# Kernel tuning notes

Measured on AMD Instinct MI355X. Metric: run time of the kernel, lower is better.

## Reference

```python
import jax, jax.numpy as jnp
import numpy as np

B = 16384       # batch of weight blocks
IN = 64         # input_size == e_dim
DENC = 512      # dim_encoder
NRES = 2        # n_resblock (weights shared, see ResidualStack [block]*n)
NE = 2048       # n_embeddings
P = 12          # basis vectors per block
BETA = 0.25
SCALE = 1.0
SHIFT = 0.0


def setup_inputs() -> dict:
    key = jax.random.key(0)
    ks = jax.random.split(key, 6)
    s = 0.02
    return {
        "x": jax.random.normal(ks[0], (B, IN), dtype=jnp.float32),
        "enc_w1": jax.random.normal(ks[1], (IN, DENC), dtype=jnp.float32) * s,
        "enc_b1": jnp.zeros((DENC,), jnp.float32),
        "res_w": jax.random.normal(ks[2], (DENC, DENC), dtype=jnp.float32) * s,
        "res_b": jnp.zeros((DENC,), jnp.float32),
        "res_g": jnp.ones((DENC,), jnp.float32),
        "res_beta": jnp.zeros((DENC,), jnp.float32),
        "enc_w2": jax.random.normal(ks[3], (DENC, IN * P), dtype=jnp.float32) * s,
        "enc_b2": jnp.zeros((IN * P,), jnp.float32),
        "emb": jax.random.uniform(ks[4], (NE, IN), jnp.float32, -1.0 / NE, 1.0 / NE),
    }


def _layer_norm(r, g, b):
    mu = jnp.mean(r, axis=-1, keepdims=True)
    var = jnp.mean((r - mu) ** 2, axis=-1, keepdims=True)
    return (r - mu) * jax.lax.rsqrt(var + 1e-5) * g + b


def reference(x, enc_w1, enc_b1, res_w, res_b, res_g, res_beta, enc_w2, enc_b2, emb):
    sg = jax.lax.stop_gradient
    x_shift = (x - SHIFT) / SCALE

    # encoder: Linear -> (shared ResBlock) x NRES -> Linear
    h = x_shift @ enc_w1 + enc_b1                      # (B, DENC)
    for _ in range(NRES):
        h = h + jax.nn.relu(_layer_norm(h @ res_w + res_b, res_g, res_beta))
    z = h @ enc_w2 + enc_b2                            # (B, P*IN)

    z_e = z.reshape(B, P, IN)
    zf = z_e.reshape(-1, IN)                           # (B*P, IN)

    # pairwise squared distances to codebook, argmin, gather
    d = (jnp.sum(zf ** 2, axis=1, keepdims=True)
         + jnp.sum(emb ** 2, axis=1)
         - 2.0 * zf @ emb.T)                           # (B*P, NE)
    idx = jnp.argmin(d, axis=1)                        # (B*P,)
    z_q = emb[idx].reshape(B, P, IN)

    loss = (jnp.mean((sg(z_q) - z_e) ** 2)
            + BETA * jnp.mean((z_q - sg(z_e)) ** 2))

    # straight-through estimator
    z_q = z_e + sg(z_q - z_e)

    counts = jnp.zeros((NE,), jnp.float32).at[idx].add(1.0) / idx.shape[0]
    perplexity = jnp.exp(-jnp.sum(counts * jnp.log(counts + 1e-10)))

    # pinv-based reconstruction: A (B, IN, P), coeff = pinv(A) @ x_shift
    A = jnp.transpose(z_q, (0, 2, 1))                  # (B, IN, P)
    coeff = jnp.matmul(jnp.linalg.pinv(A), x_shift[..., None])  # (B, P, 1)
    x_hat = jnp.matmul(A, coeff)[..., 0]               # (B, IN)
    x_hat = SCALE * x_hat + SHIFT

    return (loss, x_hat, perplexity, idx, coeff)
```

## Files before the change

kernel.cpp:

```cpp
#include <hip/hip_runtime.h>
#include <math.h>

#define B_    16384
#define IN_   64
#define DENC_ 512
#define NE_   2048
#define P_    12
#define ROWS_ 196608
#define BETA_ 0.25

#define XHAT_OFF 1
#define PERP_OFF 1048577
#define IDXF_OFF 1048578
#define COEF_OFF 1245186

typedef __bf16 bf16x8 __attribute__((ext_vector_type(8)));
typedef float  f32x16 __attribute__((ext_vector_type(16)));

__device__ __forceinline__ void split3(float v, __bf16& h, __bf16& m, __bf16& l) {
    h = (__bf16)v;
    float r1 = v - (float)h;
    m = (__bf16)r1;
    float r2 = r1 - (float)m;
    l = (__bf16)r2;
}

__global__ void k_wsplit(const float* __restrict__ W,
                         __bf16* __restrict__ Wh, __bf16* __restrict__ Wm,
                         __bf16* __restrict__ Wl, int kshift, int N, int total) {
    int idx = blockIdx.x * 256 + threadIdx.x;
    if (idx < total) {
        int n = idx >> kshift;
        int k = idx & ((1 << kshift) - 1);
        float v = W[(size_t)k * N + n];
        __bf16 h, m, l;
        split3(v, h, m, l);
        Wh[idx] = h; Wm[idx] = m; Wl[idx] = l;
    }
}

__global__ __launch_bounds__(256) void k_gemm_mfma(const float* __restrict__ A,
                                                   const __bf16* __restrict__ Bh,
                                                   const __bf16* __restrict__ Bm,
                                                   const __bf16* __restrict__ Bl,
                                                   const float* __restrict__ bias,
                                                   float* __restrict__ C,
                                                   int N, int K) {
    __shared__ __bf16 eS[3][64 * 64];

    const int tid = threadIdx.x;
    const int w = tid >> 6, lane = tid & 63;
    const int r0 = blockIdx.y * 128 + w * 32;
    const int n0 = blockIdx.x * 64;
    const int lrow = lane & 31;
    const int half = lane >> 5;

    f32x16 acc0, acc1;
#pragma unroll
    for (int i = 0; i < 16; ++i) { acc0[i] = 0.0f; acc1[i] = 0.0f; }

    for (int k0 = 0; k0 < K; k0 += 64) {
        __syncthreads();
        {
            const int col = tid >> 3, q = tid & 7;
#pragma unroll
            for (int p = 0; p < 2; ++p) {
                int cc = col + 32 * p;
                int g = q ^ (cc & 7);
                size_t soff = (size_t)(n0 + cc) * K + k0 + q * 8;
                int doff = cc * 64 + g * 8;
                *(float4*)(&eS[0][doff]) = *(const float4*)(Bh + soff);
                *(float4*)(&eS[1][doff]) = *(const float4*)(Bm + soff);
                *(float4*)(&eS[2][doff]) = *(const float4*)(Bl + soff);
            }
        }
        __syncthreads();

        bf16x8 ah[4], am[4], al[4];
        {
            const float* ar = A + (size_t)(r0 + lrow) * K + k0 + half * 8;
#pragma unroll
            for (int kc = 0; kc < 4; ++kc) {
                float4 u0 = *(const float4*)(ar + kc * 16);
                float4 u1 = *(const float4*)(ar + kc * 16 + 4);
                float v[8] = {u0.x, u0.y, u0.z, u0.w, u1.x, u1.y, u1.z, u1.w};
#pragma unroll
                for (int j = 0; j < 8; ++j) {
                    __bf16 hh, mm, ll;
                    split3(v[j], hh, mm, ll);
                    ah[kc][j] = hh; am[kc][j] = mm; al[kc][j] = ll;
                }
            }
        }

#pragma unroll
        for (int kc = 0; kc < 4; ++kc) {
            const int q = kc * 2 + half;
            const int g = (q ^ (lrow & 7)) * 8;
            bf16x8 b0h = *(const bf16x8*)(&eS[0][lrow * 64 + g]);
            bf16x8 b0m = *(const bf16x8*)(&eS[1][lrow * 64 + g]);
            bf16x8 b0l = *(const bf16x8*)(&eS[2][lrow * 64 + g]);
            bf16x8 b1h = *(const bf16x8*)(&eS[0][(lrow + 32) * 64 + g]);
            bf16x8 b1m = *(const bf16x8*)(&eS[1][(lrow + 32) * 64 + g]);
            bf16x8 b1l = *(const bf16x8*)(&eS[2][(lrow + 32) * 64 + g]);

            acc0 = __builtin_amdgcn_mfma_f32_32x32x16_bf16(ah[kc], b0h, acc0, 0, 0, 0);
            acc1 = __builtin_amdgcn_mfma_f32_32x32x16_bf16(ah[kc], b1h, acc1, 0, 0, 0);
            acc0 = __builtin_amdgcn_mfma_f32_32x32x16_bf16(ah[kc], b0m, acc0, 0, 0, 0);
            acc1 = __builtin_amdgcn_mfma_f32_32x32x16_bf16(ah[kc], b1m, acc1, 0, 0, 0);
            acc0 = __builtin_amdgcn_mfma_f32_32x32x16_bf16(am[kc], b0h, acc0, 0, 0, 0);
            acc1 = __builtin_amdgcn_mfma_f32_32x32x16_bf16(am[kc], b1h, acc1, 0, 0, 0);
            acc0 = __builtin_amdgcn_mfma_f32_32x32x16_bf16(ah[kc], b0l, acc0, 0, 0, 0);
            acc1 = __builtin_amdgcn_mfma_f32_32x32x16_bf16(ah[kc], b1l, acc1, 0, 0, 0);
            acc0 = __builtin_amdgcn_mfma_f32_32x32x16_bf16(am[kc], b0m, acc0, 0, 0, 0);
            acc1 = __builtin_amdgcn_mfma_f32_32x32x16_bf16(am[kc], b1m, acc1, 0, 0, 0);
            acc0 = __builtin_amdgcn_mfma_f32_32x32x16_bf16(al[kc], b0h, acc0, 0, 0, 0);
            acc1 = __builtin_amdgcn_mfma_f32_32x32x16_bf16(al[kc], b1h, acc1, 0, 0, 0);
        }
    }

    const int col0 = n0 + lrow, col1 = col0 + 32;
    const float bv0 = bias[col0], bv1 = bias[col1];
#pragma unroll
    for (int r = 0; r < 16; ++r) {
        int row = r0 + (r & 3) + 8 * (r >> 2) + 4 * half;
        C[(size_t)row * N + col0] = acc0[r] + bv0;
        C[(size_t)row * N + col1] = acc1[r] + bv1;
    }
}

__global__ __launch_bounds__(256) void k_lnrelu(const float* __restrict__ t,
                                                float* __restrict__ h,
                                                const float* __restrict__ g,
                                                const float* __restrict__ beta) {
    const int tid = threadIdx.x;
    const int wv = tid >> 6, lane = tid & 63;
    const int row = blockIdx.x * 4 + wv;
    const float* tr = t + (size_t)row * DENC_;
    float* hr = h + (size_t)row * DENC_;

    float4 v0 = *(const float4*)(tr + lane * 4);
    float4 v1 = *(const float4*)(tr + 256 + lane * 4);

    float s = v0.x + v0.y + v0.z + v0.w + v1.x + v1.y + v1.z + v1.w;
#pragma unroll
    for (int m = 1; m < 64; m <<= 1) s += __shfl_xor(s, m);
    float mu = s / 512.0f;

    float d0x = v0.x - mu, d0y = v0.y - mu, d0z = v0.z - mu, d0w = v0.w - mu;
    float d1x = v1.x - mu, d1y = v1.y - mu, d1z = v1.z - mu, d1w = v1.w - mu;
    float vs = d0x * d0x + d0y * d0y + d0z * d0z + d0w * d0w +
               d1x * d1x + d1y * d1y + d1z * d1z + d1w * d1w;
#pragma unroll
    for (int m = 1; m < 64; m <<= 1) vs += __shfl_xor(vs, m);
    float var = vs / 512.0f;
    float rs = (float)(1.0 / sqrt((double)var + 1e-5));

    float4 g0 = *(const float4*)(g + lane * 4);
    float4 g1 = *(const float4*)(g + 256 + lane * 4);
    float4 b0 = *(const float4*)(beta + lane * 4);
    float4 b1 = *(const float4*)(beta + 256 + lane * 4);

    float4 h0 = *(float4*)(hr + lane * 4);
    float4 h1 = *(float4*)(hr + 256 + lane * 4);

    h0.x += fmaxf(d0x * rs * g0.x + b0.x, 0.0f);
    h0.y += fmaxf(d0y * rs * g0.y + b0.y, 0.0f);
    h0.z += fmaxf(d0z * rs * g0.z + b0.z, 0.0f);
    h0.w += fmaxf(d0w * rs * g0.w + b0.w, 0.0f);
    h1.x += fmaxf(d1x * rs * g1.x + b1.x, 0.0f);
    h1.y += fmaxf(d1y * rs * g1.y + b1.y, 0.0f);
    h1.z += fmaxf(d1z * rs * g1.z + b1.z, 0.0f);
    h1.w += fmaxf(d1w * rs * g1.w + b1.w, 0.0f);

    *(float4*)(hr + lane * 4) = h0;
    *(float4*)(hr + 256 + lane * 4) = h1;
}

__global__ void k_esplit(const float* __restrict__ emb, float* __restrict__ se,
                         __bf16* __restrict__ Ehi, __bf16* __restrict__ Emid,
                         __bf16* __restrict__ Elo) {
    int c = blockIdx.x * 256 + threadIdx.x;
    if (c < NE_) {
        float s = 0.0f;
        for (int k = 0; k < 64; ++k) {
            float v = emb[(size_t)c * 64 + k];
            s += v * v;
            __bf16 h, m, l;
            split3(v, h, m, l);
            Ehi[(size_t)c * 64 + k] = h;
            Emid[(size_t)c * 64 + k] = m;
            Elo[(size_t)c * 64 + k] = l;
        }
        se[c] = s;
    }
}

__global__ __launch_bounds__(256) void k_rowsq(const float* __restrict__ z,
                                               float* __restrict__ sz) {
    const int tid = threadIdx.x;
    const int row = blockIdx.x * 64 + (tid >> 2);
    const int part = tid & 3;
    const float4* zp = (const float4*)(z + (size_t)row * 64) + part * 4;
    float s = 0.0f;
#pragma unroll
    for (int i = 0; i < 4; ++i) {
        float4 v = zp[i];
        s += v.x * v.x + v.y * v.y + v.z * v.z + v.w * v.w;
    }
    s += __shfl_xor(s, 1);
    s += __shfl_xor(s, 2);
    if (part == 0) sz[row] = s;
}

__global__ __launch_bounds__(256) void k_distm(const float* __restrict__ z,
                                               const float* __restrict__ se,
                                               const float* __restrict__ sz,
                                               const __bf16* __restrict__ Ehi,
                                               const __bf16* __restrict__ Emid,
                                               const __bf16* __restrict__ Elo,
                                               int* __restrict__ idxw,
                                               float* __restrict__ idxf,
                                               float* __restrict__ dminw,
                                               int* __restrict__ counts) {
    __shared__ __bf16 eS[3][64 * 64];

    const int tid = threadIdx.x;
    const int w = tid >> 6, lane = tid & 63;
    const int r0 = blockIdx.x * 128 + w * 32;
    const int lrow = lane & 31;
    const int half = lane >> 5;

    bf16x8 ah[4], am[4], al[4];
    {
        const float* zr = z + (size_t)(r0 + lrow) * 64 + half * 8;
#pragma unroll
        for (int kc = 0; kc < 4; ++kc) {
            float4 u0 = *(const float4*)(zr + kc * 16);
            float4 u1 = *(const float4*)(zr + kc * 16 + 4);
            float v[8] = {u0.x, u0.y, u0.z, u0.w, u1.x, u1.y, u1.z, u1.w};
#pragma unroll
            for (int j = 0; j < 8; ++j) {
                __bf16 hh, mm, ll;
                split3(v[j], hh, mm, ll);
                ah[kc][j] = hh; am[kc][j] = mm; al[kc][j] = ll;
            }
        }
    }

    float szv[16];
#pragma unroll
    for (int r = 0; r < 16; ++r) {
        int rl = (r & 3) + 8 * (r >> 2) + 4 * half;
        szv[r] = sz[r0 + rl];
    }

    float bd[16];
    int bi[16];
#pragma unroll
    for (int r = 0; r < 16; ++r) { bd[r] = 1e30f; bi[r] = 0; }

    for (int ch = 0; ch < 32; ++ch) {
        const int c0 = ch * 64;
        __syncthreads();
        {
            const int col = tid >> 3, q = tid & 7;
#pragma unroll
            for (int p = 0; p < 2; ++p) {
                int cc = col + 32 * p;
                int g = q ^ (cc & 7);
                size_t soff = (size_t)(c0 + cc) * 64 + q * 8;
                int doff = cc * 64 + g * 8;
                *(float4*)(&eS[0][doff]) = *(const float4*)(Ehi + soff);
                *(float4*)(&eS[1][doff]) = *(const float4*)(Emid + soff);
                *(float4*)(&eS[2][doff]) = *(const float4*)(Elo + soff);
            }
        }
        __syncthreads();

        f32x16 acc0, acc1;
#pragma unroll
        for (int i = 0; i < 16; ++i) { acc0[i] = 0.0f; acc1[i] = 0.0f; }

#pragma unroll
        for (int kc = 0; kc < 4; ++kc) {
            const int q = kc * 2 + half;
            const int g = (q ^ (lrow & 7)) * 8;
            bf16x8 b0h = *(const bf16x8*)(&eS[0][lrow * 64 + g]);
            bf16x8 b0m = *(const bf16x8*)(&eS[1][lrow * 64 + g]);
            bf16x8 b0l = *(const bf16x8*)(&eS[2][lrow * 64 + g]);
            bf16x8 b1h = *(const bf16x8*)(&eS[0][(lrow + 32) * 64 + g]);
            bf16x8 b1m = *(const bf16x8*)(&eS[1][(lrow + 32) * 64 + g]);
            bf16x8 b1l = *(const bf16x8*)(&eS[2][(lrow + 32) * 64 + g]);

            acc0 = __builtin_amdgcn_mfma_f32_32x32x16_bf16(ah[kc], b0h, acc0, 0, 0, 0);
            acc1 = __builtin_amdgcn_mfma_f32_32x32x16_bf16(ah[kc], b1h, acc1, 0, 0, 0);
            acc0 = __builtin_amdgcn_mfma_f32_32x32x16_bf16(ah[kc], b0m, acc0, 0, 0, 0);
            acc1 = __builtin_amdgcn_mfma_f32_32x32x16_bf16(ah[kc], b1m, acc1, 0, 0, 0);
            acc0 = __builtin_amdgcn_mfma_f32_32x32x16_bf16(am[kc], b0h, acc0, 0, 0, 0);
            acc1 = __builtin_amdgcn_mfma_f32_32x32x16_bf16(am[kc], b1h, acc1, 0, 0, 0);
            acc0 = __builtin_amdgcn_mfma_f32_32x32x16_bf16(ah[kc], b0l, acc0, 0, 0, 0);
            acc1 = __builtin_amdgcn_mfma_f32_32x32x16_bf16(ah[kc], b1l, acc1, 0, 0, 0);
            acc0 = __builtin_amdgcn_mfma_f32_32x32x16_bf16(am[kc], b0m, acc0, 0, 0, 0);
            acc1 = __builtin_amdgcn_mfma_f32_32x32x16_bf16(am[kc], b1m, acc1, 0, 0, 0);
            acc0 = __builtin_amdgcn_mfma_f32_32x32x16_bf16(al[kc], b0h, acc0, 0, 0, 0);
            acc1 = __builtin_amdgcn_mfma_f32_32x32x16_bf16(al[kc], b1h, acc1, 0, 0, 0);
        }

        const float se0 = se[c0 + lrow];
        const float se1 = se[c0 + lrow + 32];
        const int   ci0 = c0 + lrow, ci1 = c0 + lrow + 32;
#pragma unroll
        for (int r = 0; r < 16; ++r) {
            float d0 = fmaf(-2.0f, acc0[r], szv[r] + se0);
            if (d0 < bd[r]) { bd[r] = d0; bi[r] = ci0; }
            float d1 = fmaf(-2.0f, acc1[r], szv[r] + se1);
            if (d1 < bd[r]) { bd[r] = d1; bi[r] = ci1; }
        }
    }

#pragma unroll
    for (int r = 0; r < 16; ++r) {
        float d = bd[r];
        int i = bi[r];
#pragma unroll
        for (int off = 1; off < 32; off <<= 1) {
            float od = __shfl_xor(d, off);
            int oi = __shfl_xor(i, off);
            if (od < d || (od == d && oi < i)) { d = od; i = oi; }
        }
        bd[r] = d; bi[r] = i;
    }

    if (lrow == 0) {
#pragma unroll
        for (int r = 0; r < 16; ++r) {
            int rl = (r & 3) + 8 * (r >> 2) + 4 * half;
            int row = r0 + rl;
            idxw[row] = bi[r];
            idxf[row] = (float)bi[r];
            dminw[row] = bd[r];
            atomicAdd(&counts[bi[r]], 1);
        }
    }
}

__global__ __launch_bounds__(1024) void k_lossperp(const float* __restrict__ dmin,
                                                   const int* __restrict__ counts,
                                                   float* __restrict__ out) {
    __shared__ double red[1024];
    const int tid = threadIdx.x;

    double s = 0.0;
    for (int i = tid; i < ROWS_; i += 1024) s += (double)dmin[i];
    red[tid] = s;
    __syncthreads();
    for (int off = 512; off > 0; off >>= 1) {
        if (tid < off) red[tid] += red[tid + off];
        __syncthreads();
    }
    if (tid == 0) out[0] = (float)(red[0] * (1.0 + BETA_) / ((double)ROWS_ * IN_));
    __syncthreads();

    double hsum = 0.0;
    for (int i = tid; i < NE_; i += 1024) {
        float p = (float)counts[i] / 196608.0f;
        float lg = logf(p + 1e-10f);
        hsum += (double)(p * lg);
    }
    red[tid] = hsum;
    __syncthreads();
    for (int off = 512; off > 0; off >>= 1) {
        if (tid < off) red[tid] += red[tid + off];
        __syncthreads();
    }
    if (tid == 0) out[PERP_OFF] = (float)exp(-red[0]);
}

__global__ __launch_bounds__(256) void k_pinv(const float* __restrict__ xin,
                                              const float* __restrict__ emb,
                                              const int* __restrict__ idxw,
                                              float* __restrict__ coeff,
                                              float* __restrict__ xhat) {
    __shared__ float aS[4][12][65];
    __shared__ float xS[4][64];
    __shared__ double GS[4][12][12];
    __shared__ double bS[4][12];
    __shared__ double uS[4][12];
    __shared__ float cS[4][12];

    const int tid = threadIdx.x;
    const int wv = tid >> 6, lane = tid & 63;
    const int b = blockIdx.x * 4 + wv;

    int my = 0;
    if (lane < 12) my = idxw[(size_t)b * 12 + lane];
    int id[12];
#pragma unroll
    for (int p = 0; p < 12; ++p) id[p] = __shfl(my, p);

    int rep = lane, mcnt = 1;
    if (lane < 12) {
        rep = -1;
        mcnt = 0;
        for (int q = 0; q < 12; ++q) {
            if (id[q] == id[lane]) {
                if (rep < 0) rep = q;
                mcnt++;
            }
        }
    }

#pragma unroll
    for (int p = 0; p < 12; ++p) aS[wv][p][lane] = emb[(size_t)id[p] * 64 + lane];
    xS[wv][lane] = xin[(size_t)b * 64 + lane];
    __syncthreads();

    for (int item = lane; item < 90; item += 64) {
        if (item < 78) {
            int j = 0, k = 0, c = item;
            for (j = 0; j < 12; ++j) {
                int cnt = 12 - j;
                if (c < cnt) { k = j + c; break; }
                c -= cnt;
            }
            double s = 0.0;
            for (int t = 0; t < 64; ++t) s += (double)aS[wv][j][t] * (double)aS[wv][k][t];
            GS[wv][j][k] = s;
            GS[wv][k][j] = s;
        } else {
            int j = item - 78;
            double s = 0.0;
            for (int t = 0; t < 64; ++t) s += (double)aS[wv][j][t] * (double)xS[wv][t];
            bS[wv][j] = s;
        }
    }
    __syncthreads();

    if (lane == 0) {
        for (int p = 0; p < 12; ++p) {
            int rp = -1;
            for (int q = 0; q < 12; ++q) {
                if (id[q] == id[p]) { rp = q; break; }
            }
            if (rp != p) {
                for (int q = 0; q < 12; ++q) {
                    GS[wv][p][q] = 0.0;
                    GS[wv][q][p] = 0.0;
                }
                GS[wv][p][p] = 1.0;
                bS[wv][p] = 0.0;
            }
        }
    }
    __syncthreads();

    for (int j = 0; j < 12; ++j) {
        if (lane == j) {
            double s = GS[wv][j][j];
            for (int k = 0; k < j; ++k) {
                double l = GS[wv][j][k];
                s -= l * l;
            }
            GS[wv][j][j] = sqrt(fmax(s, 1e-30));
        }
        __syncthreads();
        if (lane > j && lane < 12) {
            double s = GS[wv][lane][j];
            for (int k = 0; k < j; ++k) s -= GS[wv][lane][k] * GS[wv][j][k];
            GS[wv][lane][j] = s / GS[wv][j][j];
        }
        __syncthreads();
    }

    if (lane == 0) {
        double y[12];
        for (int i = 0; i < 12; ++i) {
            double s = bS[wv][i];
            for (int k = 0; k < i; ++k) s -= GS[wv][i][k] * y[k];
            y[i] = s / GS[wv][i][i];
        }
        for (int i = 11; i >= 0; --i) {
            double s = y[i];
            for (int k = i + 1; k < 12; ++k) s -= GS[wv][k][i] * uS[wv][k];
            uS[wv][i] = s / GS[wv][i][i];
        }
    }
    __syncthreads();

    if (lane < 12) {
        double c = uS[wv][rep] / (double)mcnt;
        coeff[(size_t)b * 12 + lane] = (float)c;
        cS[wv][lane] = (float)c;
    }
    __syncthreads();

    float s = 0.0f;
#pragma unroll
    for (int p = 0; p < 12; ++p) s += aS[wv][p][lane] * cS[wv][p];
    xhat[(size_t)b * 64 + lane] = s;
}


extern "C" void kernel_launch(void* const* d_in, const int* in_sizes, int n_in,
                              void* d_out, int out_size, void* d_ws, size_t ws_size,
                              hipStream_t stream) {
    const float* x        = (const float*)d_in[0];
    const float* enc_w1   = (const float*)d_in[1];
    const float* enc_b1   = (const float*)d_in[2];
    const float* res_w    = (const float*)d_in[3];
    const float* res_b    = (const float*)d_in[4];
    const float* res_g    = (const float*)d_in[5];
    const float* res_beta = (const float*)d_in[6];
    const float* enc_w2   = (const float*)d_in[7];
    const float* enc_b2   = (const float*)d_in[8];
    const float* emb      = (const float*)d_in[9];

    float* out = (float*)d_out;

    float* h  = (float*)d_ws;
    float* tz = h + (size_t)B_ * DENC_;
    float* se    = h;
    float* sz    = h + 2048;
    float* dmin  = h + 2048 + (size_t)ROWS_;
    int*   idxw  = (int*)(h + 2048 + 2 * (size_t)ROWS_);
    int*   cnts  = (int*)(h + 2048 + 3 * (size_t)ROWS_);
    __bf16* Ehi  = (__bf16*)(h + 2048 + 3 * (size_t)ROWS_ + 2048);
    __bf16* Emid = Ehi + (size_t)NE_ * 64;
    __bf16* Elo  = Emid + (size_t)NE_ * 64;
    __bf16* W1h = (__bf16*)(tz + (size_t)B_ * 768);
    __bf16* W1m = W1h + (size_t)DENC_ * IN_;
    __bf16* W1l = W1m + (size_t)DENC_ * IN_;
    __bf16* Wrh = W1l + (size_t)DENC_ * IN_;
    __bf16* Wrm = Wrh + (size_t)DENC_ * DENC_;
    __bf16* Wrl = Wrm + (size_t)DENC_ * DENC_;
    __bf16* W2h = Wrl + (size_t)DENC_ * DENC_;
    __bf16* W2m = W2h + (size_t)768 * DENC_;
    __bf16* W2l = W2m + (size_t)768 * DENC_;

    float* t = tz;
    float* z = tz;

    k_wsplit<<<(DENC_ * IN_ + 255) / 256, 256, 0, stream>>>(enc_w1, W1h, W1m, W1l, 6, DENC_, DENC_ * IN_);
    k_wsplit<<<(DENC_ * DENC_ + 255) / 256, 256, 0, stream>>>(res_w, Wrh, Wrm, Wrl, 9, DENC_, DENC_ * DENC_);
    k_wsplit<<<(768 * DENC_ + 255) / 256, 256, 0, stream>>>(enc_w2, W2h, W2m, W2l, 9, 768, 768 * DENC_);

    k_gemm_mfma<<<dim3(DENC_ / 64, B_ / 128), 256, 0, stream>>>(x, W1h, W1m, W1l, enc_b1, h, DENC_, IN_);
    for (int r = 0; r < 2; ++r) {
        k_gemm_mfma<<<dim3(DENC_ / 64, B_ / 128), 256, 0, stream>>>(h, Wrh, Wrm, Wrl, res_b, t, DENC_, DENC_);
        k_lnrelu<<<B_ / 4, 256, 0, stream>>>(t, h, res_g, res_beta);
    }
    k_gemm_mfma<<<dim3(768 / 64, B_ / 128), 256, 0, stream>>>(h, W2h, W2m, W2l, enc_b2, z, 768, DENC_);

    hipMemsetAsync(cnts, 0, NE_ * sizeof(int), stream);
    k_esplit<<<NE_ / 256, 256, 0, stream>>>(emb, se, Ehi, Emid, Elo);
    k_rowsq<<<ROWS_ / 64, 256, 0, stream>>>(z, sz);
    k_distm<<<ROWS_ / 128, 256, 0, stream>>>(z, se, sz, Ehi, Emid, Elo,
                                             idxw, out + IDXF_OFF, dmin, cnts);
    k_lossperp<<<1, 1024, 0, stream>>>(dmin, cnts, out);
    k_pinv<<<B_ / 4, 256, 0, stream>>>(x, emb, idxw, out + COEF_OFF, out + XHAT_OFF);
}
```

Before: 776.3 us.

## Retile codebook distance kernel to 64 rows per wave, fuse loss reduction

```diff
diff --git a/kernel.cpp b/kernel.cpp
--- a/kernel.cpp
+++ b/kernel.cpp
@@ -177,22 +177,29 @@
     *(float4*)(hr + 256 + lane * 4) = h1;
 }
 
-__global__ void k_esplit(const float* __restrict__ emb, float* __restrict__ se,
-                         __bf16* __restrict__ Ehi, __bf16* __restrict__ Emid,
-                         __bf16* __restrict__ Elo) {
-    int c = blockIdx.x * 256 + threadIdx.x;
-    if (c < NE_) {
+__global__ __launch_bounds__(256) void k_esplit_fast(const float* __restrict__ emb,
+                                                     __bf16* __restrict__ Ehi,
+                                                     __bf16* __restrict__ Emid,
+                                                     __bf16* __restrict__ Elo) {
+    const int wv = threadIdx.x >> 6, lane = threadIdx.x & 63;
+    const int c = blockIdx.x * 4 + wv;
+    float v = emb[(size_t)c * 64 + lane];
+    __bf16 h, m, l;
+    split3(v, h, m, l);
+    Ehi[(size_t)c * 64 + lane] = h;
+    Emid[(size_t)c * 64 + lane] = m;
+    Elo[(size_t)c * 64 + lane] = l;
+}
+
+__global__ void k_esq(const float* __restrict__ emb, float* __restrict__ se) {
+    int t = blockIdx.x * 256 + threadIdx.x;
+    if (t < NE_) {
         float s = 0.0f;
         for (int k = 0; k < 64; ++k) {
-            float v = emb[(size_t)c * 64 + k];
+            float v = emb[(size_t)t * 64 + k];
             s += v * v;
-            __bf16 h, m, l;
-            split3(v, h, m, l);
-            Ehi[(size_t)c * 64 + k] = h;
-            Emid[(size_t)c * 64 + k] = m;
-            Elo[(size_t)c * 64 + k] = l;
-        }
-        se[c] = s;
+        }
+        se[t] = s;
     }
 }
 
@@ -221,19 +228,20 @@
                                                const __bf16* __restrict__ Elo,
                                                int* __restrict__ idxw,
                                                float* __restrict__ idxf,
-                                               float* __restrict__ dminw,
+                                               float* __restrict__ lossacc,
                                                int* __restrict__ counts) {
     __shared__ __bf16 eS[3][64 * 64];
 
     const int tid = threadIdx.x;
     const int w = tid >> 6, lane = tid & 63;
-    const int r0 = blockIdx.x * 128 + w * 32;
+    const int r0 = blockIdx.x * 256 + w * 64;
     const int lrow = lane & 31;
     const int half = lane >> 5;
 
-    bf16x8 ah[4], am[4], al[4];
-    {
-        const float* zr = z + (size_t)(r0 + lrow) * 64 + half * 8;
+    bf16x8 ah[2][4], am[2][4], al[2][4];
+#pragma unroll
+    for (int rg = 0; rg < 2; ++rg) {
+        const float* zr = z + (size_t)(r0 + rg * 32 + lrow) * 64 + half * 8;
 #pragma unroll
         for (int kc = 0; kc < 4; ++kc) {
             float4 u0 = *(const float4*)(zr + kc * 16);
@@ -243,25 +251,29 @@
             for (int j = 0; j < 8; ++j) {
                 __bf16 hh, mm, ll;
                 split3(v[j], hh, mm, ll);
-                ah[kc][j] = hh; am[kc][j] = mm; al[kc][j] = ll;
-            }
-        }
-    }
-
-    float szv[16];
-#pragma unroll
-    for (int r = 0; r < 16; ++r) {
-        int rl = (r & 3) + 8 * (r >> 2) + 4 * half;
-        szv[r] = sz[r0 + rl];
-    }
-
-    float bd[16];
-    int bi[16];
-#pragma unroll
-    for (int r = 0; r < 16; ++r) { bd[r] = 1e30f; bi[r] = 0; }
-
-    for (int ch = 0; ch < 32; ++ch) {
-        const int c0 = ch * 64;
+                ah[rg][kc][j] = hh; am[rg][kc][j] = mm; al[rg][kc][j] = ll;
+            }
+        }
+    }
+
+    float szv[2][16];
+#pragma unroll
+    for (int rg = 0; rg < 2; ++rg)
+#pragma unroll
+        for (int r = 0; r < 16; ++r) {
+            int rl = (r & 3) + 8 * (r >> 2) + 4 * half;
+            szv[rg][r] = sz[r0 + rg * 32 + rl];
+        }
+
+    float bd[2][16];
+    int bi[2][16];
+#pragma unroll
+    for (int rg = 0; rg < 2; ++rg)
+#pragma unroll
+        for (int r = 0; r < 16; ++r) { bd[rg][r] = 1e30f; bi[rg][r] = 0; }
+
+    for (int ch32 = 0; ch32 < 32; ++ch32) {
+        const int c0 = ch32 * 64;
         __syncthreads();
         {
             const int col = tid >> 3, q = tid & 7;
@@ -278,103 +290,100 @@
         }
         __syncthreads();
 
-        f32x16 acc0, acc1;
-#pragma unroll
-        for (int i = 0; i < 16; ++i) { acc0[i] = 0.0f; acc1[i] = 0.0f; }
-
-#pragma unroll
-        for (int kc = 0; kc < 4; ++kc) {
-            const int q = kc * 2 + half;
-            const int g = (q ^ (lrow & 7)) * 8;
-            bf16x8 b0h = *(const bf16x8*)(&eS[0][lrow * 64 + g]);
-            bf16x8 b0m = *(const bf16x8*)(&eS[1][lrow * 64 + g]);
-            bf16x8 b0l = *(const bf16x8*)(&eS[2][lrow * 64 + g]);
-            bf16x8 b1h = *(const bf16x8*)(&eS[0][(lrow + 32) * 64 + g]);
-            bf16x8 b1m = *(const bf16x8*)(&eS[1][(lrow + 32) * 64 + g]);
-            bf16x8 b1l = *(const bf16x8*)(&eS[2][(lrow + 32) * 64 + g]);
-
-            acc0 = __builtin_amdgcn_mfma_f32_32x32x16_bf16(ah[kc], b0h, acc0, 0, 0, 0);
-            acc1 = __builtin_amdgcn_mfma_f32_32x32x16_bf16(ah[kc], b1h, acc1, 0, 0, 0);
-            acc0 = __builtin_amdgcn_mfma_f32_32x32x16_bf16(ah[kc], b0m, acc0, 0, 0, 0);
-            acc1 = __builtin_amdgcn_mfma_f32_32x32x16_bf16(ah[kc], b1m, acc1, 0, 0, 0);
-            acc0 = __builtin_amdgcn_mfma_f32_32x32x16_bf16(am[kc], b0h, acc0, 0, 0, 0);
-            acc1 = __builtin_amdgcn_mfma_f32_32x32x16_bf16(am[kc], b1h, acc1, 0, 0, 0);
-            acc0 = __builtin_amdgcn_mfma_f32_32x32x16_bf16(ah[kc], b0l, acc0, 0, 0, 0);
-            acc1 = __builtin_amdgcn_mfma_f32_32x32x16_bf16(ah[kc], b1l, acc1, 0, 0, 0);
-            acc0 = __builtin_amdgcn_mfma_f32_32x32x16_bf16(am[kc], b0m, acc0, 0, 0, 0);
-            acc1 = __builtin_amdgcn_mfma_f32_32x32x16_bf16(am[kc], b1m, acc1, 0, 0, 0);
-            acc0 = __builtin_amdgcn_mfma_f32_32x32x16_bf16(al[kc], b0h, acc0, 0, 0, 0);
-            acc1 = __builtin_amdgcn_mfma_f32_32x32x16_bf16(al[kc], b1h, acc1, 0, 0, 0);
-        }
-
-        const float se0 = se[c0 + lrow];
-        const float se1 = se[c0 + lrow + 32];
-        const int   ci0 = c0 + lrow, ci1 = c0 + lrow + 32;
+#pragma unroll
+        for (int ch = 0; ch < 2; ++ch) {
+            f32x16 acc0, acc1;
+#pragma unroll
+            for (int i = 0; i < 16; ++i) { acc0[i] = 0.0f; acc1[i] = 0.0f; }
+
+            const int cL = ch * 32 + lrow;
+#pragma unroll
+            for (int kc = 0; kc < 4; ++kc) {
+                const int q = kc * 2 + half;
+                const int base = cL * 64 + (q ^ (cL & 7)) * 8;
+                bf16x8 bh = *(const bf16x8*)(&eS[0][base]);
+                acc0 = __builtin_amdgcn_mfma_f32_32x32x16_bf16(ah[0][kc], bh, acc0, 0, 0, 0);
+                acc1 = __builtin_amdgcn_mfma_f32_32x32x16_bf16(ah[1][kc], bh, acc1, 0, 0, 0);
+                acc0 = __builtin_amdgcn_mfma_f32_32x32x16_bf16(am[0][kc], bh, acc0, 0, 0, 0);
+                acc1 = __builtin_amdgcn_mfma_f32_32x32x16_bf16(am[1][kc], bh, acc1, 0, 0, 0);
+                acc0 = __builtin_amdgcn_mfma_f32_32x32x16_bf16(al[0][kc], bh, acc0, 0, 0, 0);
+                acc1 = __builtin_amdgcn_mfma_f32_32x32x16_bf16(al[1][kc], bh, acc1, 0, 0, 0);
+                bf16x8 bm = *(const bf16x8*)(&eS[1][base]);
+                acc0 = __builtin_amdgcn_mfma_f32_32x32x16_bf16(ah[0][kc], bm, acc0, 0, 0, 0);
+                acc1 = __builtin_amdgcn_mfma_f32_32x32x16_bf16(ah[1][kc], bm, acc1, 0, 0, 0);
+                acc0 = __builtin_amdgcn_mfma_f32_32x32x16_bf16(am[0][kc], bm, acc0, 0, 0, 0);
+                acc1 = __builtin_amdgcn_mfma_f32_32x32x16_bf16(am[1][kc], bm, acc1, 0, 0, 0);
+                bf16x8 bl = *(const bf16x8*)(&eS[2][base]);
+                acc0 = __builtin_amdgcn_mfma_f32_32x32x16_bf16(ah[0][kc], bl, acc0, 0, 0, 0);
+                acc1 = __builtin_amdgcn_mfma_f32_32x32x16_bf16(ah[1][kc], bl, acc1, 0, 0, 0);
+            }
+
+            const int c = c0 + cL;
+            const float sec = se[c];
+#pragma unroll
+            for (int r = 0; r < 16; ++r) {
+                float d0 = fmaf(-2.0f, acc0[r], szv[0][r] + sec);
+                if (d0 < bd[0][r]) { bd[0][r] = d0; bi[0][r] = c; }
+                float d1 = fmaf(-2.0f, acc1[r], szv[1][r] + sec);
+                if (d1 < bd[1][r]) { bd[1][r] = d1; bi[1][r] = c; }
+            }
+        }
+    }
+
+#pragma unroll
+    for (int rg = 0; rg < 2; ++rg)
 #pragma unroll
         for (int r = 0; r < 16; ++r) {
-            float d0 = fmaf(-2.0f, acc0[r], szv[r] + se0);
-            if (d0 < bd[r]) { bd[r] = d0; bi[r] = ci0; }
-            float d1 = fmaf(-2.0f, acc1[r], szv[r] + se1);
-            if (d1 < bd[r]) { bd[r] = d1; bi[r] = ci1; }
-        }
-    }
-
-#pragma unroll
-    for (int r = 0; r < 16; ++r) {
-        float d = bd[r];
-        int i = bi[r];
-#pragma unroll
-        for (int off = 1; off < 32; off <<= 1) {
-            float od = __shfl_xor(d, off);
-            int oi = __shfl_xor(i, off);
-            if (od < d || (od == d && oi < i)) { d = od; i = oi; }
-        }
-        bd[r] = d; bi[r] = i;
-    }
+            float d = bd[rg][r];
+            int i = bi[rg][r];
+#pragma unroll
+            for (int off = 1; off < 32; off <<= 1) {
+                float od = __shfl_xor(d, off);
+                int oi = __shfl_xor(i, off);
+                if (od < d || (od == d && oi < i)) { d = od; i = oi; }
+            }
+            bd[rg][r] = d; bi[rg][r] = i;
+        }
 
     if (lrow == 0) {
-#pragma unroll
-        for (int r = 0; r < 16; ++r) {
-            int rl = (r & 3) + 8 * (r >> 2) + 4 * half;
-            int row = r0 + rl;
-            idxw[row] = bi[r];
-            idxf[row] = (float)bi[r];
-            dminw[row] = bd[r];
-            atomicAdd(&counts[bi[r]], 1);
-        }
-    }
-}
-
-__global__ __launch_bounds__(1024) void k_lossperp(const float* __restrict__ dmin,
-                                                   const int* __restrict__ counts,
-                                                   float* __restrict__ out) {
-    __shared__ double red[1024];
+        float lsum = 0.0f;
+#pragma unroll
+        for (int rg = 0; rg < 2; ++rg)
+#pragma unroll
+            for (int r = 0; r < 16; ++r) {
+                int rl = (r & 3) + 8 * (r >> 2) + 4 * half;
+                int row = r0 + rg * 32 + rl;
+                idxw[row] = bi[rg][r];
+                idxf[row] = (float)bi[rg][r];
+                lsum += bd[rg][r];
+                atomicAdd(&counts[bi[rg][r]], 1);
+            }
+        atomicAdd(lossacc, lsum);
+    }
+}
+
+__global__ __launch_bounds__(256) void k_lossperp(const float* __restrict__ lossacc,
+                                                  const int* __restrict__ counts,
+                                                  float* __restrict__ out) {
+    __shared__ double red[256];
     const int tid = threadIdx.x;
 
-    double s = 0.0;
-    for (int i = tid; i < ROWS_; i += 1024) s += (double)dmin[i];
-    red[tid] = s;
-    __syncthreads();
-    for (int off = 512; off > 0; off >>= 1) {
-        if (tid < off) red[tid] += red[tid + off];
-        __syncthreads();
-    }
-    if (tid == 0) out[0] = (float)(red[0] * (1.0 + BETA_) / ((double)ROWS_ * IN_));
-    __syncthreads();
-
     double hsum = 0.0;
-    for (int i = tid; i < NE_; i += 1024) {
+    for (int i = tid; i < NE_; i += 256) {
         float p = (float)counts[i] / 196608.0f;
         float lg = logf(p + 1e-10f);
         hsum += (double)(p * lg);
     }
     red[tid] = hsum;
     __syncthreads();
-    for (int off = 512; off > 0; off >>= 1) {
+    for (int off = 128; off > 0; off >>= 1) {
         if (tid < off) red[tid] += red[tid + off];
         __syncthreads();
     }
-    if (tid == 0) out[PERP_OFF] = (float)exp(-red[0]);
+    if (tid == 0) {
+        out[PERP_OFF] = (float)exp(-red[0]);
+        out[0] = (float)((double)lossacc[0] * (1.0 + BETA_) / ((double)ROWS_ * IN_));
+    }
 }
 
 __global__ __launch_bounds__(256) void k_pinv(const float* __restrict__ xin,
@@ -522,10 +531,10 @@
     float* tz = h + (size_t)B_ * DENC_;
     float* se    = h;
     float* sz    = h + 2048;
-    float* dmin  = h + 2048 + (size_t)ROWS_;
-    int*   idxw  = (int*)(h + 2048 + 2 * (size_t)ROWS_);
-    int*   cnts  = (int*)(h + 2048 + 3 * (size_t)ROWS_);
-    __bf16* Ehi  = (__bf16*)(h + 2048 + 3 * (size_t)ROWS_ + 2048);
+    int*   idxw  = (int*)(h + 2048 + (size_t)ROWS_);
+    int*   cnts  = (int*)(h + 2048 + 2 * (size_t)ROWS_);
+    float* lossacc = (float*)(cnts + NE_);
+    __bf16* Ehi  = (__bf16*)(h + 2048 + 2 * (size_t)ROWS_ + 2048 + 16);
     __bf16* Emid = Ehi + (size_t)NE_ * 64;
     __bf16* Elo  = Emid + (size_t)NE_ * 64;
     __bf16* W1h = (__bf16*)(tz + (size_t)B_ * 768);
@@ -552,11 +561,12 @@
     }
     k_gemm_mfma<<<dim3(768 / 64, B_ / 128), 256, 0, stream>>>(h, W2h, W2m, W2l, enc_b2, z, 768, DENC_);
 
-    hipMemsetAsync(cnts, 0, NE_ * sizeof(int), stream);
-    k_esplit<<<NE_ / 256, 256, 0, stream>>>(emb, se, Ehi, Emid, Elo);
+    hipMemsetAsync(cnts, 0, (NE_ + 16) * sizeof(int), stream);
+    k_esplit_fast<<<NE_ / 4, 256, 0, stream>>>(emb, Ehi, Emid, Elo);
+    k_esq<<<NE_ / 256, 256, 0, stream>>>(emb, se);
     k_rowsq<<<ROWS_ / 64, 256, 0, stream>>>(z, sz);
-    k_distm<<<ROWS_ / 128, 256, 0, stream>>>(z, se, sz, Ehi, Emid, Elo,
-                                             idxw, out + IDXF_OFF, dmin, cnts);
-    k_lossperp<<<1, 1024, 0, stream>>>(dmin, cnts, out);
+    k_distm<<<ROWS_ / 256, 256, 0, stream>>>(z, se, sz, Ehi, Emid, Elo,
+                                             idxw, out + IDXF_OFF, lossacc, cnts);
+    k_lossperp<<<1, 256, 0, stream>>>(lossacc, cnts, out);
     k_pinv<<<B_ / 4, 256, 0, stream>>>(x, emb, idxw, out + COEF_OFF, out + XHAT_OFF);
 }
```

After: 919.1 us. 1.18x slower.

## Double-buffer GEMM and distance B-tiles with direct global-to-LDS loads

Applied to the files above, without the earlier changes.

```diff
diff --git a/kernel.cpp b/kernel.cpp
--- a/kernel.cpp
+++ b/kernel.cpp
@@ -23,6 +23,11 @@
     m = (__bf16)r1;
     float r2 = r1 - (float)m;
     l = (__bf16)r2;
+}
+
+__device__ __forceinline__ void gload_lds16(const void* g, void* l) {
+    __builtin_amdgcn_global_load_lds((const __attribute__((address_space(1))) void*)g,
+                                     (__attribute__((address_space(3))) void*)l, 16, 0, 0);
 }
 
 __global__ void k_wsplit(const float* __restrict__ W,
@@ -46,7 +51,7 @@
                                                    const float* __restrict__ bias,
                                                    float* __restrict__ C,
                                                    int N, int K) {
-    __shared__ __bf16 eS[3][64 * 64];
+    __shared__ __bf16 eS[2][3][64 * 64];
 
     const int tid = threadIdx.x;
     const int w = tid >> 6, lane = tid & 63;
@@ -55,30 +60,47 @@
     const int lrow = lane & 31;
     const int half = lane >> 5;
 
+    const int cc0 = tid >> 3, qq = tid & 7;
+    const int cc1 = cc0 + 32;
+    const size_t off0 = (size_t)cc0 * K + (size_t)((qq ^ (cc0 & 7)) * 8);
+    const size_t off1 = (size_t)cc1 * K + (size_t)((qq ^ (cc1 & 7)) * 8);
+    const size_t nbase = (size_t)n0 * K;
+    const int ld0 = w * 512;
+    const int ld1 = 2048 + w * 512;
+
     f32x16 acc0, acc1;
 #pragma unroll
     for (int i = 0; i < 16; ++i) { acc0[i] = 0.0f; acc1[i] = 0.0f; }
 
-    for (int k0 = 0; k0 < K; k0 += 64) {
+    {
+        const size_t b = nbase;
+        gload_lds16(Bh + b + off0, &eS[0][0][ld0]);
+        gload_lds16(Bh + b + off1, &eS[0][0][ld1]);
+        gload_lds16(Bm + b + off0, &eS[0][1][ld0]);
+        gload_lds16(Bm + b + off1, &eS[0][1][ld1]);
+        gload_lds16(Bl + b + off0, &eS[0][2][ld0]);
+        gload_lds16(Bl + b + off1, &eS[0][2][ld1]);
+    }
+
+    const int nch = K >> 6;
+    for (int ch = 0; ch < nch; ++ch) {
+        const int cur = ch & 1;
         __syncthreads();
-        {
-            const int col = tid >> 3, q = tid & 7;
-#pragma unroll
-            for (int p = 0; p < 2; ++p) {
-                int cc = col + 32 * p;
-                int g = q ^ (cc & 7);
-                size_t soff = (size_t)(n0 + cc) * K + k0 + q * 8;
-                int doff = cc * 64 + g * 8;
-                *(float4*)(&eS[0][doff]) = *(const float4*)(Bh + soff);
-                *(float4*)(&eS[1][doff]) = *(const float4*)(Bm + soff);
-                *(float4*)(&eS[2][doff]) = *(const float4*)(Bl + soff);
-            }
-        }
-        __syncthreads();
+
+        if (ch + 1 < nch) {
+            const int nxt = cur ^ 1;
+            const size_t b = nbase + (size_t)(ch + 1) * 64;
+            gload_lds16(Bh + b + off0, &eS[nxt][0][ld0]);
+            gload_lds16(Bh + b + off1, &eS[nxt][0][ld1]);
+            gload_lds16(Bm + b + off0, &eS[nxt][1][ld0]);
+            gload_lds16(Bm + b + off1, &eS[nxt][1][ld1]);
+            gload_lds16(Bl + b + off0, &eS[nxt][2][ld0]);
+            gload_lds16(Bl + b + off1, &eS[nxt][2][ld1]);
+        }
 
         bf16x8 ah[4], am[4], al[4];
         {
-            const float* ar = A + (size_t)(r0 + lrow) * K + k0 + half * 8;
+            const float* ar = A + (size_t)(r0 + lrow) * K + ch * 64 + half * 8;
 #pragma unroll
             for (int kc = 0; kc < 4; ++kc) {
                 float4 u0 = *(const float4*)(ar + kc * 16);
@@ -97,12 +119,12 @@
         for (int kc = 0; kc < 4; ++kc) {
             const int q = kc * 2 + half;
             const int g = (q ^ (lrow & 7)) * 8;
-            bf16x8 b0h = *(const bf16x8*)(&eS[0][lrow * 64 + g]);
-            bf16x8 b0m = *(const bf16x8*)(&eS[1][lrow * 64 + g]);
-            bf16x8 b0l = *(const bf16x8*)(&eS[2][lrow * 64 + g]);
-            bf16x8 b1h = *(const bf16x8*)(&eS[0][(lrow + 32) * 64 + g]);
-            bf16x8 b1m = *(const bf16x8*)(&eS[1][(lrow + 32) * 64 + g]);
-            bf16x8 b1l = *(const bf16x8*)(&eS[2][(lrow + 32) * 64 + g]);
+            bf16x8 b0h = *(const bf16x8*)(&eS[cur][0][lrow * 64 + g]);
+            bf16x8 b0m = *(const bf16x8*)(&eS[cur][1][lrow * 64 + g]);
+            bf16x8 b0l = *(const bf16x8*)(&eS[cur][2][lrow * 64 + g]);
+            bf16x8 b1h = *(const bf16x8*)(&eS[cur][0][(lrow + 32) * 64 + g]);
+            bf16x8 b1m = *(const bf16x8*)(&eS[cur][1][(lrow + 32) * 64 + g]);
+            bf16x8 b1l = *(const bf16x8*)(&eS[cur][2][(lrow + 32) * 64 + g]);
 
             acc0 = __builtin_amdgcn_mfma_f32_32x32x16_bf16(ah[kc], b0h, acc0, 0, 0, 0);
             acc1 = __builtin_amdgcn_mfma_f32_32x32x16_bf16(ah[kc], b1h, acc1, 0, 0, 0);
@@ -177,22 +199,29 @@
     *(float4*)(hr + 256 + lane * 4) = h1;
 }
 
-__global__ void k_esplit(const float* __restrict__ emb, float* __restrict__ se,
-                         __bf16* __restrict__ Ehi, __bf16* __restrict__ Emid,
-                         __bf16* __restrict__ Elo) {
-    int c = blockIdx.x * 256 + threadIdx.x;
-    if (c < NE_) {
+__global__ __launch_bounds__(256) void k_esplit_fast(const float* __restrict__ emb,
+                                                     __bf16* __restrict__ Ehi,
+                                                     __bf16* __restrict__ Emid,
+                                                     __bf16* __restrict__ Elo) {
+    const int wv = threadIdx.x >> 6, lane = threadIdx.x & 63;
+    const int c = blockIdx.x * 4 + wv;
+    float v = emb[(size_t)c * 64 + lane];
+    __bf16 h, m, l;
+    split3(v, h, m, l);
+    Ehi[(size_t)c * 64 + lane] = h;
+    Emid[(size_t)c * 64 + lane] = m;
+    Elo[(size_t)c * 64 + lane] = l;
+}
+
+__global__ void k_esq(const float* __restrict__ emb, float* __restrict__ se) {
+    int t = blockIdx.x * 256 + threadIdx.x;
+    if (t < NE_) {
         float s = 0.0f;
         for (int k = 0; k < 64; ++k) {
-            float v = emb[(size_t)c * 64 + k];
+            float v = emb[(size_t)t * 64 + k];
             s += v * v;
-            __bf16 h, m, l;
-            split3(v, h, m, l);
-            Ehi[(size_t)c * 64 + k] = h;
-            Emid[(size_t)c * 64 + k] = m;
-            Elo[(size_t)c * 64 + k] = l;
-        }
-        se[c] = s;
+        }
+        se[t] = s;
     }
 }
 
@@ -221,9 +250,9 @@
                                                const __bf16* __restrict__ Elo,
                                                int* __restrict__ idxw,
                                                float* __restrict__ idxf,
-                                               float* __restrict__ dminw,
+                                               float* __restrict__ lossacc,
                                                int* __restrict__ counts) {
-    __shared__ __bf16 eS[3][64 * 64];
+    __shared__ __bf16 eS[2][3][64 * 64];
 
     const int tid = threadIdx.x;
     const int w = tid >> 6, lane = tid & 63;
@@ -231,6 +260,13 @@
     const int lrow = lane & 31;
     const int half = lane >> 5;
 
+    const int cc0 = tid >> 3, qq = tid & 7;
+    const int cc1 = cc0 + 32;
+    const int off0 = cc0 * 64 + (qq ^ (cc0 & 7)) * 8;
+    const int off1 = cc1 * 64 + (qq ^ (cc1 & 7)) * 8;
+    const int ld0 = w * 512;
+    const int ld1 = 2048 + w * 512;
+
     bf16x8 ah[4], am[4], al[4];
     {
         const float* zr = z + (size_t)(r0 + lrow) * 64 + half * 8;
@@ -260,23 +296,27 @@
 #pragma unroll
     for (int r = 0; r < 16; ++r) { bd[r] = 1e30f; bi[r] = 0; }
 
+    gload_lds16(Ehi + off0, &eS[0][0][ld0]);
+    gload_lds16(Ehi + off1, &eS[0][0][ld1]);
+    gload_lds16(Emid + off0, &eS[0][1][ld0]);
+    gload_lds16(Emid + off1, &eS[0][1][ld1]);
+    gload_lds16(Elo + off0, &eS[0][2][ld0]);
+    gload_lds16(Elo + off1, &eS[0][2][ld1]);
+
     for (int ch = 0; ch < 32; ++ch) {
-        const int c0 = ch * 64;
+        const int cur = ch & 1;
         __syncthreads();
-        {
-            const int col = tid >> 3, q = tid & 7;
-#pragma unroll
-            for (int p = 0; p < 2; ++p) {
-                int cc = col + 32 * p;
-                int g = q ^ (cc & 7);
-                size_t soff = (size_t)(c0 + cc) * 64 + q * 8;
-                int doff = cc * 64 + g * 8;
-                *(float4*)(&eS[0][doff]) = *(const float4*)(Ehi + soff);
-                *(float4*)(&eS[1][doff]) = *(const float4*)(Emid + soff);
-                *(float4*)(&eS[2][doff]) = *(const float4*)(Elo + soff);
-            }
-        }
-        __syncthreads();
+
+        if (ch + 1 < 32) {
+            const int nxt = cur ^ 1;
+            const int b = (ch + 1) * 4096;
+            gload_lds16(Ehi + b + off0, &eS[nxt][0][ld0]);
+            gload_lds16(Ehi + b + off1, &eS[nxt][0][ld1]);
+            gload_lds16(Emid + b + off0, &eS[nxt][1][ld0]);
+            gload_lds16(Emid + b + off1, &eS[nxt][1][ld1]);
+            gload_lds16(Elo + b + off0, &eS[nxt][2][ld0]);
+            gload_lds16(Elo + b + off1, &eS[nxt][2][ld1]);
+        }
 
         f32x16 acc0, acc1;
 #pragma unroll
@@ -286,12 +326,12 @@
         for (int kc = 0; kc < 4; ++kc) {
             const int q = kc * 2 + half;
             const int g = (q ^ (lrow & 7)) * 8;
-            bf16x8 b0h = *(const bf16x8*)(&eS[0][lrow * 64 + g]);
-            bf16x8 b0m = *(const bf16x8*)(&eS[1][lrow * 64 + g]);
-            bf16x8 b0l = *(const bf16x8*)(&eS[2][lrow * 64 + g]);
-            bf16x8 b1h = *(const bf16x8*)(&eS[0][(lrow + 32) * 64 + g]);
-            bf16x8 b1m = *(const bf16x8*)(&eS[1][(lrow + 32) * 64 + g]);
-            bf16x8 b1l = *(const bf16x8*)(&eS[2][(lrow + 32) * 64 + g]);
+            bf16x8 b0h = *(const bf16x8*)(&eS[cur][0][lrow * 64 + g]);
+            bf16x8 b0m = *(const bf16x8*)(&eS[cur][1][lrow * 64 + g]);
+            bf16x8 b0l = *(const bf16x8*)(&eS[cur][2][lrow * 64 + g]);
+            bf16x8 b1h = *(const bf16x8*)(&eS[cur][0][(lrow + 32) * 64 + g]);
+            bf16x8 b1m = *(const bf16x8*)(&eS[cur][1][(lrow + 32) * 64 + g]);
+            bf16x8 b1l = *(const bf16x8*)(&eS[cur][2][(lrow + 32) * 64 + g]);
 
             acc0 = __builtin_amdgcn_mfma_f32_32x32x16_bf16(ah[kc], b0h, acc0, 0, 0, 0);
             acc1 = __builtin_amdgcn_mfma_f32_32x32x16_bf16(ah[kc], b1h, acc1, 0, 0, 0);
@@ -307,6 +347,7 @@
             acc1 = __builtin_amdgcn_mfma_f32_32x32x16_bf16(al[kc], b1h, acc1, 0, 0, 0);
         }
 
+        const int c0 = ch * 64;
         const float se0 = se[c0 + lrow];
         const float se1 = se[c0 + lrow + 32];
         const int   ci0 = c0 + lrow, ci1 = c0 + lrow + 32;
@@ -333,48 +374,42 @@
     }
 
     if (lrow == 0) {
+        float lsum = 0.0f;
 #pragma unroll
         for (int r = 0; r < 16; ++r) {
             int rl = (r & 3) + 8 * (r >> 2) + 4 * half;
             int row = r0 + rl;
             idxw[row] = bi[r];
             idxf[row] = (float)bi[r];
-            dminw[row] = bd[r];
+            lsum += bd[r];
             atomicAdd(&counts[bi[r]], 1);
         }
-    }
-}
-
-__global__ __launch_bounds__(1024) void k_lossperp(const float* __restrict__ dmin,
-                                                   const int* __restrict__ counts,
-                                                   float* __restrict__ out) {
-    __shared__ double red[1024];
+        atomicAdd(lossacc, lsum);
+    }
+}
+
+__global__ __launch_bounds__(256) void k_lossperp(const float* __restrict__ lossacc,
+                                                  const int* __restrict__ counts,
+                                                  float* __restrict__ out) {
+    __shared__ double red[256];
     const int tid = threadIdx.x;
 
-    double s = 0.0;
-    for (int i = tid; i < ROWS_; i += 1024) s += (double)dmin[i];
-    red[tid] = s;
-    __syncthreads();
-    for (int off = 512; off > 0; off >>= 1) {
-        if (tid < off) red[tid] += red[tid + off];
-        __syncthreads();
-    }
-    if (tid == 0) out[0] = (float)(red[0] * (1.0 + BETA_) / ((double)ROWS_ * IN_));
-    __syncthreads();
-
     double hsum = 0.0;
-    for (int i = tid; i < NE_; i += 1024) {
+    for (int i = tid; i < NE_; i += 256) {
         float p = (float)counts[i] / 196608.0f;
         float lg = logf(p + 1e-10f);
         hsum += (double)(p * lg);
     }
     red[tid] = hsum;
     __syncthreads();
-    for (int off = 512; off > 0; off >>= 1) {
+    for (int off = 128; off > 0; off >>= 1) {
         if (tid < off) red[tid] += red[tid + off];
         __syncthreads();
     }
-    if (tid == 0) out[PERP_OFF] = (float)exp(-red[0]);
+    if (tid == 0) {
+        out[PERP_OFF] = (float)exp(-red[0]);
+        out[0] = (float)((double)lossacc[0] * (1.0 + BETA_) / ((double)ROWS_ * IN_));
+    }
 }
 
 __global__ __launch_bounds__(256) void k_pinv(const float* __restrict__ xin,
@@ -522,10 +557,10 @@
     float* tz = h + (size_t)B_ * DENC_;
     float* se    = h;
     float* sz    = h + 2048;
-    float* dmin  = h + 2048 + (size_t)ROWS_;
-    int*   idxw  = (int*)(h + 2048 + 2 * (size_t)ROWS_);
-    int*   cnts  = (int*)(h + 2048 + 3 * (size_t)ROWS_);
-    __bf16* Ehi  = (__bf16*)(h + 2048 + 3 * (size_t)ROWS_ + 2048);
+    int*   idxw  = (int*)(h + 2048 + (size_t)ROWS_);
+    int*   cnts  = (int*)(h + 2048 + 2 * (size_t)ROWS_);
+    float* lossacc = (float*)(cnts + NE_);
+    __bf16* Ehi  = (__bf16*)(h + 2048 + 2 * (size_t)ROWS_ + 2048 + 16);
     __bf16* Emid = Ehi + (size_t)NE_ * 64;
     __bf16* Elo  = Emid + (size_t)NE_ * 64;
     __bf16* W1h = (__bf16*)(tz + (size_t)B_ * 768);
@@ -552,11 +587,12 @@
     }
     k_gemm_mfma<<<dim3(768 / 64, B_ / 128), 256, 0, stream>>>(h, W2h, W2m, W2l, enc_b2, z, 768, DENC_);
 
-    hipMemsetAsync(cnts, 0, NE_ * sizeof(int), stream);
-    k_esplit<<<NE_ / 256, 256, 0, stream>>>(emb, se, Ehi, Emid, Elo);
+    hipMemsetAsync(cnts, 0, (NE_ + 16) * sizeof(int), stream);
+    k_esplit_fast<<<NE_ / 4, 256, 0, stream>>>(emb, Ehi, Emid, Elo);
+    k_esq<<<NE_ / 256, 256, 0, stream>>>(emb, se);
     k_rowsq<<<ROWS_ / 64, 256, 0, stream>>>(z, sz);
     k_distm<<<ROWS_ / 128, 256, 0, stream>>>(z, se, sz, Ehi, Emid, Elo,
-                                             idxw, out + IDXF_OFF, dmin, cnts);
-    k_lossperp<<<1, 1024, 0, stream>>>(dmin, cnts, out);
+                                             idxw, out + IDXF_OFF, lossacc, cnts);
+    k_lossperp<<<1, 256, 0, stream>>>(lossacc, cnts, out);
     k_pinv<<<B_ / 4, 256, 0, stream>>>(x, emb, idxw, out + COEF_OFF, out + XHAT_OFF);
 }
```

New measurement: 763.4 us. Within noise of the previous version (-1.7%).
